# Kernel tuning notes

Measured on AMD Instinct MI355X. Metric: run time of the kernel, lower is better.

## Reference

```python
import jax, jax.numpy as jnp
import numpy as np

B, N, D = 16, 1024, 320
L, H, K = 256, 256, 5
PAIR_IN = 2 * D + 6 + L  # 902


def setup_inputs() -> dict:
    key = jax.random.key(0)
    ks = jax.random.split(key, 8)
    return {
        "object_features": jax.random.normal(ks[0], (B, N, D), jnp.float32),
        "language_embedding": jax.random.normal(ks[1], (B, L), jnp.float32),
        "centers": jax.random.normal(ks[2], (B, N, 3), jnp.float32),
        "sizes": jax.random.uniform(ks[3], (B, N, 3), jnp.float32),
        "object_mask": jnp.ones((B, N), dtype=bool),
        "W1": jax.random.normal(ks[4], (PAIR_IN, H), jnp.float32) * 0.02,
        "b1": jnp.zeros((H,), jnp.float32),
        "W2": jax.random.normal(ks[5], (H, 1), jnp.float32) * 0.02,
        "b2": jnp.zeros((1,), jnp.float32),
    }


def _gather_neighbors(x, idx):
    # x: [B, N, C], idx: [B, N, k] -> [B, N, k, C]
    b, n, c = x.shape
    k = idx.shape[-1]
    flat = jnp.take_along_axis(x, idx.reshape(b, n * k)[..., None], axis=1)
    return flat.reshape(b, n, k, c)


def reference(object_features, language_embedding, centers, sizes, object_mask,
              W1, b1, W2, b2):
    b, n, d = object_features.shape
    k = min(K, n - 1)
    # pairwise squared distances [B, N, N]
    diff = centers[:, :, None, :] - centers[:, None, :, :]
    dist = jnp.sum(diff * diff, axis=-1)
    pair_mask = object_mask[:, :, None] & object_mask[:, None, :]
    dist = jnp.where(pair_mask, dist, jnp.inf)
    dist = jnp.where(jnp.eye(n, dtype=bool)[None], jnp.inf, dist)
    # k nearest neighbors (smallest distance)
    _, neighbor_indices = jax.lax.top_k(-dist, k)  # [B, N, k]

    neighbor_feats = _gather_neighbors(object_features, neighbor_indices)  # [B,N,k,D]
    neighbor_centers = _gather_neighbors(centers, neighbor_indices)        # [B,N,k,3]
    neighbor_sizes = _gather_neighbors(sizes, neighbor_indices)            # [B,N,k,3]

    rel_pos = (centers[:, :, None, :] - neighbor_centers) / 5.0
    rel_size = (sizes[:, :, None, :] - neighbor_sizes) / 2.0

    feat_i = jnp.broadcast_to(object_features[:, :, None, :], (b, n, k, d))
    lang = jnp.broadcast_to(language_embedding[:, None, None, :], (b, n, k, language_embedding.shape[-1]))
    pair_input = jnp.concatenate([feat_i, neighbor_feats, rel_pos, rel_size, lang], axis=-1)

    # relation MLP (dropout is identity in eval)
    h = jax.nn.relu(jnp.einsum('bnkp,ph->bnkh', pair_input, W1) + b1)
    scores = (jnp.einsum('bnkh,ho->bnko', h, W2) + b2)[..., 0]  # [B,N,k]
    weights = jax.nn.softmax(scores, axis=2)

    context = jnp.einsum('bnk,bnkd->bnd', weights, neighbor_feats)
    enhanced = object_features + context  # use_residual=True
    return enhanced, weights, neighbor_indices
```

## Files before the change

### kernel.cpp

```cpp
#include <hip/hip_runtime.h>
#include <math.h>

#define NB 16
#define NN 1024
#define ND 320
#define NL 256
#define NH 256
#define NK 5
#define KE 352

typedef short bf16x8 __attribute__((ext_vector_type(8)));
typedef float f32x4 __attribute__((ext_vector_type(4)));
typedef unsigned long long u64;

__device__ inline ushort f2bf(float f) {
    unsigned u = __float_as_uint(f);
    u += 0x7fff + ((u >> 16) & 1);
    return (ushort)(u >> 16);
}
__device__ inline float bf2f(ushort u) {
    return __uint_as_float(((unsigned)u) << 16);
}

__global__ __launch_bounds__(256) void mini_prep_kernel(const float* __restrict__ W1,
                                                        ushort* __restrict__ W1T,
                                                        const float* __restrict__ lang,
                                                        const float* __restrict__ b1,
                                                        float* __restrict__ LP) {
    __shared__ float red[4][64];
    int bid = blockIdx.x;
    if (bid < 512) {
        int n = bid;
        int rowbase = (n < 256) ? 0 : 320;
        int col = n & 255;
        float sign = (n < 256) ? 1.f : -1.f;
        for (int k = threadIdx.x; k < KE; k += 256) {
            float v;
            if (k < 320) v = W1[(rowbase + k) * NH + col];
            else if (k < 326) v = sign * W1[(640 + (k - 320)) * NH + col];
            else v = 0.f;
            W1T[n * KE + k] = f2bf(v);
        }
        return;
    }
    int id = bid - 512;
    int b = id >> 2, hq = id & 3;
    int w = threadIdx.x >> 6, lane = threadIdx.x & 63;
    int h = hq * 64 + lane;
    const float* lb = lang + b * NL;
    float acc = 0.f;
    int l0 = w * 64;
#pragma unroll 8
    for (int l = 0; l < 64; ++l)
        acc = fmaf(lb[l0 + l], W1[(646 + l0 + l) * NH + h], acc);
    red[w][lane] = acc;
    __syncthreads();
    if (w == 0)
        LP[b * NH + h] = b1[h] + red[0][lane] + red[1][lane]
                       + red[2][lane] + red[3][lane];
}

#define LDP 40
__global__ __launch_bounds__(256) void mfma_gemm_kernel(const float* __restrict__ A32,
                                                        const float* __restrict__ C3,
                                                        const float* __restrict__ S3,
                                                        const ushort* __restrict__ BT,
                                                        ushort* __restrict__ P) {
    __shared__ ushort Als[128 * LDP];
    __shared__ ushort Bls[128 * LDP];
    int t = threadIdx.x;
    int lane = t & 63;
    int w = t >> 6;
    int wrow = (w >> 1) * 64, wcol = (w & 1) * 64;
    int m0 = blockIdx.x * 128, n0 = blockIdx.y * 128;
    int lr = lane & 15;
    int lg = lane >> 4;

    f32x4 zero = {0.f, 0.f, 0.f, 0.f};
    f32x4 acc[4][4];
#pragma unroll
    for (int i = 0; i < 4; ++i)
#pragma unroll
        for (int j = 0; j < 4; ++j) acc[i][j] = zero;

    for (int ks = 0; ks < 11; ++ks) {
        int k0 = ks * 32;
#pragma unroll
        for (int it = 0; it < 2; ++it) {
            int s = it * 256 + t;
            int r = s >> 2, q = s & 3;
            int4 pk;
            if (ks < 10) {
                const float* src = &A32[(m0 + r) * ND + k0 + q * 8];
                float4 v0 = *(const float4*)src;
                float4 v1 = *(const float4*)(src + 4);
                pk.x = (int)f2bf(v0.x) | ((int)f2bf(v0.y) << 16);
                pk.y = (int)f2bf(v0.z) | ((int)f2bf(v0.w) << 16);
                pk.z = (int)f2bf(v1.x) | ((int)f2bf(v1.y) << 16);
                pk.w = (int)f2bf(v1.z) | ((int)f2bf(v1.w) << 16);
            } else {
                pk.x = 0; pk.y = 0; pk.z = 0; pk.w = 0;
                if (q == 0) {
                    int m = m0 + r;
                    float c0 = C3[m * 3 + 0] * 0.2f;
                    float c1 = C3[m * 3 + 1] * 0.2f;
                    float c2 = C3[m * 3 + 2] * 0.2f;
                    float s0 = S3[m * 3 + 0] * 0.5f;
                    float s1 = S3[m * 3 + 1] * 0.5f;
                    float s2 = S3[m * 3 + 2] * 0.5f;
                    pk.x = (int)f2bf(c0) | ((int)f2bf(c1) << 16);
                    pk.y = (int)f2bf(c2) | ((int)f2bf(s0) << 16);
                    pk.z = (int)f2bf(s1) | ((int)f2bf(s2) << 16);
                }
            }
            *(int4*)&Als[r * LDP + q * 8] = pk;
            *(int4*)&Bls[r * LDP + q * 8] =
                *(const int4*)&BT[(n0 + r) * KE + k0 + q * 8];
        }
        __syncthreads();
        bf16x8 af[4], bfr[4];
#pragma unroll
        for (int i = 0; i < 4; ++i) {
            af[i]  = *(bf16x8*)&Als[(wrow + i * 16 + lr) * LDP + lg * 8];
            bfr[i] = *(bf16x8*)&Bls[(wcol + i * 16 + lr) * LDP + lg * 8];
        }
#pragma unroll
        for (int i = 0; i < 4; ++i)
#pragma unroll
            for (int j = 0; j < 4; ++j)
                acc[i][j] = __builtin_amdgcn_mfma_f32_16x16x32_bf16(af[i], bfr[j],
                                                                    acc[i][j], 0, 0, 0);
        __syncthreads();
    }

#pragma unroll
    for (int i = 0; i < 4; ++i) {
#pragma unroll
        for (int j = 0; j < 4; ++j) {
            int col = n0 + wcol + j * 16 + lr;
#pragma unroll
            for (int e = 0; e < 4; ++e) {
                int row = m0 + wrow + i * 16 + lg * 4 + e;
                P[row * 512 + col] = f2bf(acc[i][j][e]);
            }
        }
    }
}

#define INS(d, j, D0, D1, D2, D3, D4, I0, I1, I2, I3, I4)                      \
    {                                                                          \
        bool c0 = d < D0, c1 = d < D1, c2 = d < D2, c3 = d < D3, c4 = d < D4;  \
        D4 = c4 ? (c3 ? D3 : d) : D4;  I4 = c4 ? (c3 ? I3 : j) : I4;           \
        D3 = c3 ? (c2 ? D2 : d) : D3;  I3 = c3 ? (c2 ? I2 : j) : I3;           \
        D2 = c2 ? (c1 ? D1 : d) : D2;  I2 = c2 ? (c1 ? I1 : j) : I2;           \
        D1 = c1 ? (c0 ? D0 : d) : D1;  I1 = c1 ? (c0 ? I0 : j) : I1;           \
        D0 = c0 ? d : D0;              I0 = c0 ? j : I0;                       \
    }

__device__ inline u64 packdi(float d, int i) {
    return ((u64)__float_as_uint(d) << 32) | (unsigned)i;
}

__global__ __launch_bounds__(256) void knn_score_kernel(const float* __restrict__ feats,
                                                        const float* __restrict__ centers,
                                                        const ushort* __restrict__ P,
                                                        const float* __restrict__ LP,
                                                        const float* __restrict__ W2,
                                                        float* __restrict__ enhanced,
                                                        float* __restrict__ weights,
                                                        float* __restrict__ idx_f) {
    __shared__ float cxs[NN], cys[NN], czs[NN];
    int wave = threadIdx.x >> 6;
    int lane = threadIdx.x & 63;
    int sbid = (blockIdx.x & 7) * 256 + (blockIdx.x >> 3);
    int wv = sbid * 4 + wave;
    int rowA = wv * 2, rowB = rowA | 1;
    int b = rowA >> 10;
    int iA = rowA & (NN - 1), iB = iA + 1;

    const float* cbase = centers + b * (NN * 3);
    for (int j = threadIdx.x; j < NN; j += 256) {
        int o = j * 3;
        cxs[j] = cbase[o]; cys[j] = cbase[o + 1]; czs[j] = cbase[o + 2];
    }
    __syncthreads();

    float pxA = cxs[iA], pyA = cys[iA], pzA = czs[iA];
    float pxB = cxs[iB], pyB = cys[iB], pzB = czs[iB];

    float dA0 = INFINITY, dA1 = INFINITY, dA2 = INFINITY, dA3 = INFINITY, dA4 = INFINITY;
    float dB0 = INFINITY, dB1 = INFINITY, dB2 = INFINITY, dB3 = INFINITY, dB4 = INFINITY;
    int iA0 = -1, iA1 = -1, iA2 = -1, iA3 = -1, iA4 = -1;
    int iB0 = -1, iB1 = -1, iB2 = -1, iB3 = -1, iB4 = -1;

#pragma unroll
    for (int tt = 0; tt < 16; ++tt) {
        int j = tt * 64 + lane;
        float cx = cxs[j], cy = cys[j], cz = czs[j];
        float dxA = pxA - cx, dyA = pyA - cy, dzA = pzA - cz;
        float dA = fmaf(dzA, dzA, fmaf(dyA, dyA, dxA * dxA));
        dA = (j == iA) ? INFINITY : dA;
        float dxB = pxB - cx, dyB = pyB - cy, dzB = pzB - cz;
        float dB = fmaf(dzB, dzB, fmaf(dyB, dyB, dxB * dxB));
        dB = (j == iB) ? INFINITY : dB;
        INS(dA, j, dA0, dA1, dA2, dA3, dA4, iA0, iA1, iA2, iA3, iA4);
        INS(dB, j, dB0, dB1, dB2, dB3, dB4, iB0, iB1, iB2, iB3, iB4);
    }

    int jnA[NK], jnB[NK];
#pragma unroll
    for (int k = 0; k < NK; ++k) {
        u64 mA = packdi(dA0, iA0);
        u64 mB = packdi(dB0, iB0);
#pragma unroll
        for (int off = 32; off > 0; off >>= 1) {
            u64 oA = __shfl_xor(mA, off);
            u64 oB = __shfl_xor(mB, off);
            mA = (oA < mA) ? oA : mA;
            mB = (oB < mB) ? oB : mB;
        }
        int mjA = (int)(unsigned)mA;
        int mjB = (int)(unsigned)mB;
        jnA[k] = mjA;
        jnB[k] = mjB;
        bool cA = (iA0 == mjA);
        dA0 = cA ? dA1 : dA0;  iA0 = cA ? iA1 : iA0;
        dA1 = cA ? dA2 : dA1;  iA1 = cA ? iA2 : iA1;
        dA2 = cA ? dA3 : dA2;  iA2 = cA ? iA3 : iA2;
        dA3 = cA ? dA4 : dA3;  iA3 = cA ? iA4 : iA3;
        dA4 = cA ? INFINITY : dA4;
        bool cB = (iB0 == mjB);
        dB0 = cB ? dB1 : dB0;  iB0 = cB ? iB1 : iB0;
        dB1 = cB ? dB2 : dB1;  iB1 = cB ? iB2 : iB1;
        dB2 = cB ? dB3 : dB2;  iB2 = cB ? iB3 : iB2;
        dB3 = cB ? dB4 : dB3;  iB3 = cB ? iB4 : iB3;
        dB4 = cB ? INFINITY : dB4;
    }

    if (lane == 0) {
#pragma unroll
        for (int k = 0; k < NK; ++k) {
            idx_f[rowA * NK + k] = (float)jnA[k];
            idx_f[rowB * NK + k] = (float)jnB[k];
        }
    }

    float4 lpv = ((const float4*)LP)[b * 64 + lane];
    ushort4 pfA = *(const ushort4*)&P[rowA * 512 + (lane << 2)];
    ushort4 pfB = *(const ushort4*)&P[rowB * 512 + (lane << 2)];
    float4 baseA = make_float4(bf2f(pfA.x) + lpv.x, bf2f(pfA.y) + lpv.y,
                               bf2f(pfA.z) + lpv.z, bf2f(pfA.w) + lpv.w);
    float4 baseB = make_float4(bf2f(pfB.x) + lpv.x, bf2f(pfB.y) + lpv.y,
                               bf2f(pfB.z) + lpv.z, bf2f(pfB.w) + lpv.w);
    float4 w2v = ((const float4*)W2)[lane];

    int pbase = (b << 10) * 512 + 256 + (lane << 2);
    float pA[NK], pB[NK];
#pragma unroll
    for (int k = 0; k < NK; ++k) {
        ushort4 pnA = *(const ushort4*)&P[pbase + jnA[k] * 512];
        ushort4 pnB = *(const ushort4*)&P[pbase + jnB[k] * 512];
        float hx = fmaxf(baseA.x + bf2f(pnA.x), 0.f);
        float hy = fmaxf(baseA.y + bf2f(pnA.y), 0.f);
        float hz = fmaxf(baseA.z + bf2f(pnA.z), 0.f);
        float hw = fmaxf(baseA.w + bf2f(pnA.w), 0.f);
        pA[k] = hx * w2v.x + hy * w2v.y + hz * w2v.z + hw * w2v.w;
        hx = fmaxf(baseB.x + bf2f(pnB.x), 0.f);
        hy = fmaxf(baseB.y + bf2f(pnB.y), 0.f);
        hz = fmaxf(baseB.z + bf2f(pnB.z), 0.f);
        hw = fmaxf(baseB.w + bf2f(pnB.w), 0.f);
        pB[k] = hx * w2v.x + hy * w2v.y + hz * w2v.z + hw * w2v.w;
    }

#pragma unroll
    for (int off = 32; off > 0; off >>= 1) {
        pA[0] += __shfl_xor(pA[0], off);
        pA[1] += __shfl_xor(pA[1], off);
        pA[2] += __shfl_xor(pA[2], off);
        pA[3] += __shfl_xor(pA[3], off);
        pA[4] += __shfl_xor(pA[4], off);
        pB[0] += __shfl_xor(pB[0], off);
        pB[1] += __shfl_xor(pB[1], off);
        pB[2] += __shfl_xor(pB[2], off);
        pB[3] += __shfl_xor(pB[3], off);
        pB[4] += __shfl_xor(pB[4], off);
    }

    float wkA[NK], wkB[NK];
    {
        float mxA = pA[0], mxB = pB[0];
#pragma unroll
        for (int k = 1; k < NK; ++k) { mxA = fmaxf(mxA, pA[k]); mxB = fmaxf(mxB, pB[k]); }
        float sA = 0.f, sB = 0.f;
#pragma unroll
        for (int k = 0; k < NK; ++k) {
            wkA[k] = __expf(pA[k] - mxA); sA += wkA[k];
            wkB[k] = __expf(pB[k] - mxB); sB += wkB[k];
        }
        float ivA = 1.f / sA, ivB = 1.f / sB;
#pragma unroll
        for (int k = 0; k < NK; ++k) { wkA[k] *= ivA; wkB[k] *= ivB; }
    }

    if (lane == 0) {
#pragma unroll
        for (int k = 0; k < NK; ++k) {
            weights[rowA * NK + k] = wkA[k];
            weights[rowB * NK + k] = wkB[k];
        }
    }

    const float* fb = feats + b * (NN * ND);
    {
        int dA_ = rowA * ND + (lane << 2);
        int dB_ = rowB * ND + (lane << 2);
        float4 aA = *(const float4*)&feats[dA_];
        float4 aB = *(const float4*)&feats[dB_];
#pragma unroll
        for (int k = 0; k < NK; ++k) {
            float4 nA = *(const float4*)&fb[jnA[k] * ND + (lane << 2)];
            float4 nB = *(const float4*)&fb[jnB[k] * ND + (lane << 2)];
            aA.x = fmaf(wkA[k], nA.x, aA.x); aA.y = fmaf(wkA[k], nA.y, aA.y);
            aA.z = fmaf(wkA[k], nA.z, aA.z); aA.w = fmaf(wkA[k], nA.w, aA.w);
            aB.x = fmaf(wkB[k], nB.x, aB.x); aB.y = fmaf(wkB[k], nB.y, aB.y);
            aB.z = fmaf(wkB[k], nB.z, aB.z); aB.w = fmaf(wkB[k], nB.w, aB.w);
        }
        *(float4*)&enhanced[dA_] = aA;
        *(float4*)&enhanced[dB_] = aB;
    }
    if (lane < 16) {
        int d0 = 256 + (lane << 2);
        float4 aA = *(const float4*)&feats[rowA * ND + d0];
        float4 aB = *(const float4*)&feats[rowB * ND + d0];
#pragma unroll
        for (int k = 0; k < NK; ++k) {
            float4 nA = *(const float4*)&fb[jnA[k] * ND + d0];
            float4 nB = *(const float4*)&fb[jnB[k] * ND + d0];
            aA.x = fmaf(wkA[k], nA.x, aA.x); aA.y = fmaf(wkA[k], nA.y, aA.y);
            aA.z = fmaf(wkA[k], nA.z, aA.z); aA.w = fmaf(wkA[k], nA.w, aA.w);
            aB.x = fmaf(wkB[k], nB.x, aB.x); aB.y = fmaf(wkB[k], nB.y, aB.y);
            aB.z = fmaf(wkB[k], nB.z, aB.z); aB.w = fmaf(wkB[k], nB.w, aB.w);
        }
        *(float4*)&enhanced[rowA * ND + d0] = aA;
        *(float4*)&enhanced[rowB * ND + d0] = aB;
    }
}

extern "C" void kernel_launch(void* const* d_in, const int* in_sizes, int n_in,
                              void* d_out, int out_size, void* d_ws, size_t ws_size,
                              hipStream_t stream) {
    const float* feats   = (const float*)d_in[0];
    const float* lang    = (const float*)d_in[1];
    const float* centers = (const float*)d_in[2];
    const float* sizes   = (const float*)d_in[3];
    const float* W1 = (const float*)d_in[5];
    const float* b1 = (const float*)d_in[6];
    const float* W2 = (const float*)d_in[7];

    float* out = (float*)d_out;
    float* enhanced = out;
    float* weights  = out + (size_t)NB * NN * ND;
    float* idx_f    = weights + (size_t)NB * NN * NK;

    char* ws = (char*)d_ws;
    ushort* P   = (ushort*)ws;
    ushort* W1T = (ushort*)(ws + 16777216);
    float*  LP  = (float*)(ws + 16777216 + 360448);

    mini_prep_kernel<<<dim3(576), 256, 0, stream>>>(W1, W1T, lang, b1, LP);
    mfma_gemm_kernel<<<dim3(128, 4), 256, 0, stream>>>(feats, centers, sizes, W1T, P);
    knn_score_kernel<<<dim3(2048), 256, 0, stream>>>(feats, centers, P, LP,
                                                     W2, enhanced, weights, idx_f);
}
```

Measured before the change: 53.66 us.

## Load GEMM B tile via direct global-to-LDS and hoist score-phase loads

The GEMM kernel now streams the bf16 weight tile straight from global memory into LDS with global_load_lds, skipping the register round trip. The B tile loses its padding, which may add LDS bank conflicts on the MFMA fragment reads. In the kNN kernel, the P, LP and W2 loads move ahead of the neighbor search so their latency overlaps the distance computation. The top-k merge now keeps packed 64-bit distance/index keys, which cuts per-step selects but keeps more 64-bit values in registers.

After: 54.76 us. 2.0% more time.

```diff
diff --git a/kernel.cpp b/kernel.cpp
--- a/kernel.cpp
+++ b/kernel.cpp
@@ -67,7 +67,7 @@
                                                         const ushort* __restrict__ BT,
                                                         ushort* __restrict__ P) {
     __shared__ ushort Als[128 * LDP];
-    __shared__ ushort Bls[128 * LDP];
+    __shared__ ushort Bls[128 * 32];
     int t = threadIdx.x;
     int lane = t & 63;
     int w = t >> 6;
@@ -89,6 +89,14 @@
         for (int it = 0; it < 2; ++it) {
             int s = it * 256 + t;
             int r = s >> 2, q = s & 3;
+            {
+                const ushort* gsrc = &BT[(n0 + r) * KE + k0 + q * 8];
+                char* ldst = (char*)Bls + it * 4096 + w * 1024;
+                __builtin_amdgcn_global_load_lds(
+                    (const __attribute__((address_space(1))) unsigned*)gsrc,
+                    (__attribute__((address_space(3))) unsigned*)ldst,
+                    16, 0, 0);
+            }
             int4 pk;
             if (ks < 10) {
                 const float* src = &A32[(m0 + r) * ND + k0 + q * 8];
@@ -114,15 +122,13 @@
                 }
             }
             *(int4*)&Als[r * LDP + q * 8] = pk;
-            *(int4*)&Bls[r * LDP + q * 8] =
-                *(const int4*)&BT[(n0 + r) * KE + k0 + q * 8];
         }
         __syncthreads();
         bf16x8 af[4], bfr[4];
 #pragma unroll
         for (int i = 0; i < 4; ++i) {
             af[i]  = *(bf16x8*)&Als[(wrow + i * 16 + lr) * LDP + lg * 8];
-            bfr[i] = *(bf16x8*)&Bls[(wcol + i * 16 + lr) * LDP + lg * 8];
+            bfr[i] = *(bf16x8*)&Bls[(wcol + i * 16 + lr) * 32 + lg * 8];
         }
 #pragma unroll
         for (int i = 0; i < 4; ++i)
@@ -160,6 +166,7 @@
 __device__ inline u64 packdi(float d, int i) {
     return ((u64)__float_as_uint(d) << 32) | (unsigned)i;
 }
+#define PACK_INF 0x7F800000FFFFFFFFull
 
 __global__ __launch_bounds__(256) void knn_score_kernel(const float* __restrict__ feats,
                                                         const float* __restrict__ centers,
@@ -178,6 +185,11 @@
     int b = rowA >> 10;
     int iA = rowA & (NN - 1), iB = iA + 1;
 
+    float4 lpv = ((const float4*)LP)[b * 64 + lane];
+    ushort4 pfA = *(const ushort4*)&P[rowA * 512 + (lane << 2)];
+    ushort4 pfB = *(const ushort4*)&P[rowB * 512 + (lane << 2)];
+    float4 w2v = ((const float4*)W2)[lane];
+
     const float* cbase = centers + b * (NN * 3);
     for (int j = threadIdx.x; j < NN; j += 256) {
         int o = j * 3;
@@ -207,11 +219,16 @@
         INS(dB, j, dB0, dB1, dB2, dB3, dB4, iB0, iB1, iB2, iB3, iB4);
     }
 
+    u64 vA0 = packdi(dA0, iA0), vA1 = packdi(dA1, iA1), vA2 = packdi(dA2, iA2),
+        vA3 = packdi(dA3, iA3), vA4 = packdi(dA4, iA4);
+    u64 vB0 = packdi(dB0, iB0), vB1 = packdi(dB1, iB1), vB2 = packdi(dB2, iB2),
+        vB3 = packdi(dB3, iB3), vB4 = packdi(dB4, iB4);
+
     int jnA[NK], jnB[NK];
 #pragma unroll
     for (int k = 0; k < NK; ++k) {
-        u64 mA = packdi(dA0, iA0);
-        u64 mB = packdi(dB0, iB0);
+        u64 mA = vA0;
+        u64 mB = vB0;
 #pragma unroll
         for (int off = 32; off > 0; off >>= 1) {
             u64 oA = __shfl_xor(mA, off);
@@ -219,22 +236,20 @@
             mA = (oA < mA) ? oA : mA;
             mB = (oB < mB) ? oB : mB;
         }
-        int mjA = (int)(unsigned)mA;
-        int mjB = (int)(unsigned)mB;
-        jnA[k] = mjA;
-        jnB[k] = mjB;
-        bool cA = (iA0 == mjA);
-        dA0 = cA ? dA1 : dA0;  iA0 = cA ? iA1 : iA0;
-        dA1 = cA ? dA2 : dA1;  iA1 = cA ? iA2 : iA1;
-        dA2 = cA ? dA3 : dA2;  iA2 = cA ? iA3 : iA2;
-        dA3 = cA ? dA4 : dA3;  iA3 = cA ? iA4 : iA3;
-        dA4 = cA ? INFINITY : dA4;
-        bool cB = (iB0 == mjB);
-        dB0 = cB ? dB1 : dB0;  iB0 = cB ? iB1 : iB0;
-        dB1 = cB ? dB2 : dB1;  iB1 = cB ? iB2 : iB1;
-        dB2 = cB ? dB3 : dB2;  iB2 = cB ? iB3 : iB2;
-        dB3 = cB ? dB4 : dB3;  iB3 = cB ? iB4 : iB3;
-        dB4 = cB ? INFINITY : dB4;
+        jnA[k] = (int)(unsigned)mA;
+        jnB[k] = (int)(unsigned)mB;
+        bool cA = (vA0 == mA);
+        vA0 = cA ? vA1 : vA0;
+        vA1 = cA ? vA2 : vA1;
+        vA2 = cA ? vA3 : vA2;
+        vA3 = cA ? vA4 : vA3;
+        vA4 = cA ? PACK_INF : vA4;
+        bool cB = (vB0 == mB);
+        vB0 = cB ? vB1 : vB0;
+        vB1 = cB ? vB2 : vB1;
+        vB2 = cB ? vB3 : vB2;
+        vB3 = cB ? vB4 : vB3;
+        vB4 = cB ? PACK_INF : vB4;
     }
 
     if (lane == 0) {
@@ -245,14 +260,10 @@
         }
     }
 
-    float4 lpv = ((const float4*)LP)[b * 64 + lane];
-    ushort4 pfA = *(const ushort4*)&P[rowA * 512 + (lane << 2)];
-    ushort4 pfB = *(const ushort4*)&P[rowB * 512 + (lane << 2)];
     float4 baseA = make_float4(bf2f(pfA.x) + lpv.x, bf2f(pfA.y) + lpv.y,
                                bf2f(pfA.z) + lpv.z, bf2f(pfA.w) + lpv.w);
     float4 baseB = make_float4(bf2f(pfB.x) + lpv.x, bf2f(pfB.y) + lpv.y,
                                bf2f(pfB.z) + lpv.z, bf2f(pfB.w) + lpv.w);
-    float4 w2v = ((const float4*)W2)[lane];
 
     int pbase = (b << 10) * 512 + 256 + (lane << 2);
     float pA[NK], pB[NK];
```
